# Optimization experiments

Measured on AMD Instinct MI355X. Metric: run time of the kernel, lower is better.

## Reference

```python
import jax, jax.numpy as jnp
import numpy as np

N = 100000      # nodes
E = 1600000     # edges (avg degree 16)
F_IN = 64       # input feature dim
H = 64          # hidden dim
R = 4           # relations
G = 512         # graphs in batch
C = 10          # classes
L = 3           # total conv layers (conv1 + L-1)
SCALE = 0.1


def setup_inputs() -> dict:
    key = jax.random.key(0)
    ks = jax.random.split(key, 12)
    x = jax.random.normal(ks[0], (N, F_IN), jnp.float32)
    edge_index = jax.random.randint(ks[1], (2, E), 0, N)
    edge_type = jax.random.randint(ks[2], (E,), 0, R)
    batch = jnp.sort(jax.random.randint(ks[3], (N,), 0, G))
    W1 = jax.random.normal(ks[4], (R, F_IN, H), jnp.float32) * SCALE
    root1 = jax.random.normal(ks[5], (F_IN, H), jnp.float32) * SCALE
    b1 = jnp.zeros((H,), jnp.float32)
    Wl = jax.random.normal(ks[6], (L - 1, R, H, H), jnp.float32) * SCALE
    rootl = jax.random.normal(ks[7], (L - 1, H, H), jnp.float32) * SCALE
    bl = jnp.zeros((L - 1, H), jnp.float32)
    lin1_w = jax.random.normal(ks[8], (H, H), jnp.float32) * SCALE
    lin1_b = jnp.zeros((H,), jnp.float32)
    lin2_w = jax.random.normal(ks[9], (H, C), jnp.float32) * SCALE
    lin2_b = jnp.zeros((C,), jnp.float32)
    return {"x": x, "edge_index": edge_index, "edge_type": edge_type,
            "batch": batch, "W1": W1, "root1": root1, "b1": b1,
            "Wl": Wl, "rootl": rootl, "bl": bl,
            "lin1_w": lin1_w, "lin1_b": lin1_b,
            "lin2_w": lin2_w, "lin2_b": lin2_b}


def _rgcn_conv(x, src, dst, edge_type, W, root, b):
    # Per-relation transform of all nodes (R small), then gather per edge.
    h = jnp.einsum('nd,rdf->rnf', x, W)          # [R, N, H]
    msg = h[edge_type, src]                      # [E, H] gather
    # Mean aggregation per (dst, relation): PyG RGCNConv default aggr='mean'.
    seg = dst * R + edge_type                    # combined (node, relation) id
    cnt = jax.ops.segment_sum(jnp.ones((msg.shape[0],), x.dtype), seg,
                              num_segments=x.shape[0] * R)
    norm = 1.0 / jnp.maximum(cnt[seg], 1.0)      # [E]
    agg = jax.ops.segment_sum(msg * norm[:, None], dst,
                              num_segments=x.shape[0])  # [N, H]
    return agg + x @ root + b


def _mean_pool(x, batch, num_graphs):
    s = jax.ops.segment_sum(x, batch, num_segments=num_graphs)
    cnt = jax.ops.segment_sum(jnp.ones((x.shape[0],), x.dtype), batch,
                              num_segments=num_graphs)
    return s / jnp.maximum(cnt, 1.0)[:, None]


def reference(x, edge_index, edge_type, batch, W1, root1, b1, Wl, rootl, bl,
              lin1_w, lin1_b, lin2_w, lin2_b):
    src, dst = edge_index[0], edge_index[1]
    h = jax.nn.relu(_rgcn_conv(x, src, dst, edge_type, W1, root1, b1))
    for i in range(L - 1):
        h = jax.nn.relu(_rgcn_conv(h, src, dst, edge_type, Wl[i], rootl[i], bl[i]))
    g = _mean_pool(h, batch, G)                  # [G, H]
    g = jax.nn.relu(g @ lin1_w + lin1_b)
    # dropout omitted (inference / training=False)
    return g @ lin2_w + lin2_b                   # [G, C]
```

## Files before the change

### kernel.cpp

```cpp
#include <hip/hip_runtime.h>

#define TILE 32
#define KDIM 320

typedef __attribute__((ext_vector_type(8))) short short8;
typedef __attribute__((ext_vector_type(4))) float f32x4;

__device__ inline unsigned short rne_bf16(float f) {
    union { float f; unsigned u; } x;
    x.f = f;
    unsigned r = (x.u + 0x7FFF + ((x.u >> 16) & 1)) >> 16;
    return (unsigned short)r;
}

__device__ inline float bf16_f(unsigned short v) {
    union { unsigned u; float f; } x;
    x.u = ((unsigned)v) << 16;
    return x.f;
}


__global__ void k_count(const int* __restrict__ dst, const int* __restrict__ typ,
                        int* __restrict__ cnt4, int* __restrict__ rank, int E) {
    int e = blockIdx.x * 256 + threadIdx.x;
    if (e < E) {
        int seg = dst[e] * 4 + typ[e];
        rank[e] = atomicAdd(&cnt4[seg], 1);
    }
}

__global__ void k_scan1(const int* __restrict__ in, int* __restrict__ out,
                        int* __restrict__ bsum, int M) {
    __shared__ int s[256];
    int t = threadIdx.x;
    int base = blockIdx.x * 1024 + t * 4;
    int v0 = (base + 0 < M) ? in[base + 0] : 0;
    int v1 = (base + 1 < M) ? in[base + 1] : 0;
    int v2 = (base + 2 < M) ? in[base + 2] : 0;
    int v3 = (base + 3 < M) ? in[base + 3] : 0;
    int ts = v0 + v1 + v2 + v3;
    s[t] = ts;
    __syncthreads();
    for (int off = 1; off < 256; off <<= 1) {
        int x = (t >= off) ? s[t - off] : 0;
        __syncthreads();
        s[t] += x;
        __syncthreads();
    }
    int excl = (t == 0) ? 0 : s[t - 1];
    if (t == 255) bsum[blockIdx.x] = s[255];
    if (base + 0 < M) out[base + 0] = excl;
    if (base + 1 < M) out[base + 1] = excl + v0;
    if (base + 2 < M) out[base + 2] = excl + v0 + v1;
    if (base + 3 < M) out[base + 3] = excl + v0 + v1 + v2;
}

__global__ void k_scan2(const int* __restrict__ bsum, int* __restrict__ boff, int nb) {
    __shared__ int s[512];
    int t = threadIdx.x;
    s[t] = (t < nb) ? bsum[t] : 0;
    __syncthreads();
    for (int off = 1; off < 512; off <<= 1) {
        int x = (t >= off) ? s[t - off] : 0;
        __syncthreads();
        s[t] += x;
        __syncthreads();
    }
    if (t < nb) boff[t] = (t == 0) ? 0 : s[t - 1];
}

__global__ void k_scan3(int* __restrict__ out, const int* __restrict__ boff, int M, int E) {
    int i = blockIdx.x * 256 + threadIdx.x;
    if (i < M) out[i] += boff[i >> 10];
    else if (i == M) out[M] = E;
}

__global__ void k_fill(const int* __restrict__ src, const int* __restrict__ dst,
                       const int* __restrict__ typ, const int* __restrict__ start4,
                       const int* __restrict__ rank, int* __restrict__ elist, int E) {
    int e = blockIdx.x * 256 + threadIdx.x;
    if (e < E) {
        int seg = dst[e] * 4 + typ[e];
        elist[start4[seg] + rank[e]] = src[e];
    }
}


__global__ void k_prep(const float* __restrict__ x, unsigned short* __restrict__ xb, int ncvt,
                       const float* __restrict__ W1, const float* __restrict__ root1,
                       const float* __restrict__ Wl, const float* __restrict__ rootl,
                       unsigned short* __restrict__ Wp, int nwp,
                       const int* __restrict__ batch, int* __restrict__ gstart,
                       int nN, int nG) {
    int b = blockIdx.x;
    if (b < ncvt) {
        int i = (b * 256 + threadIdx.x) * 4;
        float4 v = *reinterpret_cast<const float4*>(&x[i]);
        ushort4 o;
        o.x = rne_bf16(v.x); o.y = rne_bf16(v.y);
        o.z = rne_bf16(v.z); o.w = rne_bf16(v.w);
        *reinterpret_cast<ushort4*>(&xb[i]) = o;
        return;
    }
    b -= ncvt;
    if (b < nwp) {
        int idx = b * 256 + threadIdx.x;
        const int TOT = 3 * 320 * 64;
        if (idx >= TOT) return;
        int j = idx & 7;
        int lane = (idx >> 3) & 63;
        int t = idx >> 9;
        int ks = t % 10;
        int lnt = t / 10;
        int nt = lnt & 3;
        int layer = lnt >> 2;
        int k = ks * 32 + ((lane >> 4) << 3) + j;
        int h = nt * 16 + (lane & 15);
        float v;
        if (k < 256) {
            v = (layer == 0) ? W1[k * 64 + h] : Wl[(layer - 1) * 16384 + k * 64 + h];
        } else {
            v = (layer == 0) ? root1[(k - 256) * 64 + h]
                             : rootl[(layer - 1) * 4096 + (k - 256) * 64 + h];
        }
        Wp[idx] = rne_bf16(v);
        return;
    }
    b -= nwp;
    {
        int n = b * 256 + threadIdx.x;
        if (n >= nN) return;
        int bb = batch[n];
        if (n == 0) {
            for (int g = 0; g <= bb; ++g) gstart[g] = 0;
        } else {
            int bp = batch[n - 1];
            for (int g = bp + 1; g <= bb; ++g) gstart[g] = n;
        }
        if (n == nN - 1) {
            for (int g = bb + 1; g <= nG; ++g) gstart[g] = nN;
        }
    }
}


__global__ __launch_bounds__(256, 6) void k_conv(
        const unsigned short* __restrict__ hin, unsigned short* __restrict__ hout,
        const int* __restrict__ elist, const int* __restrict__ start4,
        const unsigned short* __restrict__ Wp, const float* __restrict__ bias, int nN) {
    __shared__ unsigned short A2[TILE * KDIM];
    const int tid = threadIdx.x;
    const int lane = tid & 63;
    const int wvs = __builtin_amdgcn_readfirstlane(tid >> 6);
    const int wv = tid >> 6;
    const int tile = blockIdx.x * TILE;

    for (int jj = 0; jj < 8; ++jj) {
        const int nl = wvs * 8 + jj;
        const int n = tile + nl;
        unsigned short* Arow = &A2[nl * KDIM];
        const int sw = (((lane >> 3) ^ (nl & 7)) << 3) + (lane & 7);
        if (n >= nN) {
#pragma unroll
            for (int seg = 0; seg < 5; ++seg) Arow[seg * 64 + sw] = 0;
            continue;
        }
        const int e0 = __builtin_amdgcn_readfirstlane(start4[n * 4 + 0]);
        const int e1 = __builtin_amdgcn_readfirstlane(start4[n * 4 + 1]);
        const int e2 = __builtin_amdgcn_readfirstlane(start4[n * 4 + 2]);
        const int e3 = __builtin_amdgcn_readfirstlane(start4[n * 4 + 3]);
        const int e4 = __builtin_amdgcn_readfirstlane(start4[n * 4 + 4]);

        unsigned short selfb = hin[((size_t)n << 6) + lane];
        float S0 = 0.f, S1 = 0.f, S2 = 0.f, S3 = 0.f;
        int p = e0;

        for (; p + 8 <= e4; p += 8) {
            int qidx[8];
#pragma unroll
            for (int u = 0; u < 8; ++u)
                qidx[u] = __builtin_amdgcn_readfirstlane(elist[p + u]);
            unsigned short vb[8];
#pragma unroll
            for (int u = 0; u < 8; ++u)
                vb[u] = hin[((size_t)qidx[u] << 6) + lane];
            __builtin_amdgcn_sched_barrier(0);
#pragma unroll
            for (int u = 0; u < 8; ++u) {
                float t = bf16_f(vb[u]);
                int q = p + u;
                S0 += t;
                S1 += (q >= e1) ? t : 0.f;
                S2 += (q >= e2) ? t : 0.f;
                S3 += (q >= e3) ? t : 0.f;
            }
        }
        if (p < e4) {
            int qidx[8];
#pragma unroll
            for (int u = 0; u < 8; ++u) {
                int q = p + u;
                int qc = (q < e4) ? q : (e4 - 1);
                qidx[u] = __builtin_amdgcn_readfirstlane(elist[qc]);
            }
            unsigned short vb[8];
#pragma unroll
            for (int u = 0; u < 8; ++u)
                vb[u] = hin[((size_t)qidx[u] << 6) + lane];
            __builtin_amdgcn_sched_barrier(0);
#pragma unroll
            for (int u = 0; u < 8; ++u) {
                int q = p + u;
                float t = (q < e4) ? bf16_f(vb[u]) : 0.f;
                S0 += t;
                S1 += (q >= e1) ? t : 0.f;
                S2 += (q >= e2) ? t : 0.f;
                S3 += (q >= e3) ? t : 0.f;
            }
        }

        int c0 = e1 - e0, c1 = e2 - e1, c2 = e3 - e2, c3 = e4 - e3;
        float a0 = (S0 - S1) * ((c0 > 0) ? 1.0f / (float)c0 : 0.f);
        float a1 = (S1 - S2) * ((c1 > 0) ? 1.0f / (float)c1 : 0.f);
        float a2 = (S2 - S3) * ((c2 > 0) ? 1.0f / (float)c2 : 0.f);
        float a3 = S3 * ((c3 > 0) ? 1.0f / (float)c3 : 0.f);
        Arow[0   + sw] = rne_bf16(a0);
        Arow[64  + sw] = rne_bf16(a1);
        Arow[128 + sw] = rne_bf16(a2);
        Arow[192 + sw] = rne_bf16(a3);
        Arow[256 + sw] = selfb;
    }
    __syncthreads();

    const int mt = wv & 1;
    const int ntb = (wv >> 1) << 1;
    const int nloc = mt * 16 + (lane & 15);
    f32x4 acc0 = {0.f, 0.f, 0.f, 0.f};
    f32x4 acc1 = {0.f, 0.f, 0.f, 0.f};
    const unsigned short* wp0 = Wp + ((size_t)(ntb * 10) * 64 + lane) * 8;
    const unsigned short* wp1 = Wp + ((size_t)((ntb + 1) * 10) * 64 + lane) * 8;
#pragma unroll 2
    for (int ks = 0; ks < 10; ++ks) {
        int kc = ks * 4 + (lane >> 4);
        int swz = (kc & ~7) | ((kc & 7) ^ (lane & 7));
        short8 a = *reinterpret_cast<const short8*>(&A2[nloc * KDIM + swz * 8]);
        short8 b0 = *reinterpret_cast<const short8*>(&wp0[ks * 512]);
        short8 b1 = *reinterpret_cast<const short8*>(&wp1[ks * 512]);
        acc0 = __builtin_amdgcn_mfma_f32_16x16x32_bf16(a, b0, acc0, 0, 0, 0);
        acc1 = __builtin_amdgcn_mfma_f32_16x16x32_bf16(a, b1, acc1, 0, 0, 0);
    }
    const int h0 = ntb * 16 + (lane & 15);
    const int nr = tile + mt * 16 + ((lane >> 4) << 2);
    const float bb0 = bias[h0];
    const float bb1 = bias[h0 + 16];
#pragma unroll
    for (int r = 0; r < 4; ++r) {
        int n = nr + r;
        if (n < nN) {
            hout[(size_t)n * 64 + h0]      = rne_bf16(fmaxf(acc0[r] + bb0, 0.f));
            hout[(size_t)n * 64 + h0 + 16] = rne_bf16(fmaxf(acc1[r] + bb1, 0.f));
        }
    }
}


__global__ void k_poolmlp(const unsigned short* __restrict__ h,
                          const int* __restrict__ gstart,
                          const float* __restrict__ w1, const float* __restrict__ b1,
                          const float* __restrict__ w2, const float* __restrict__ b2,
                          float* __restrict__ out) {
    __shared__ float red[4][64];
    __shared__ float sg[64];
    __shared__ float sh[64];
    int g = blockIdx.x;
    int t = threadIdx.x;
    int f = t & 63;
    int sl = t >> 6;
    int s = gstart[g], e = gstart[g + 1];
    float acc = 0.f;
    for (int n = s + sl; n < e; n += 4)
        acc += bf16_f(h[(size_t)n * 64 + f]);
    red[sl][f] = acc;
    __syncthreads();
    if (sl == 0) {
        int c = e - s;
        float m = (red[0][f] + red[1][f] + red[2][f] + red[3][f]) /
                  (float)((c > 0) ? c : 1);
        sg[f] = m;
    }
    __syncthreads();
    if (sl == 0) {
        float a = b1[f];
#pragma unroll 16
        for (int k = 0; k < 64; ++k) a += sg[k] * w1[k * 64 + f];
        sh[f] = fmaxf(a, 0.f);
    }
    __syncthreads();
    if (t < 10) {
        float o = b2[t];
#pragma unroll 16
        for (int k = 0; k < 64; ++k) o += sh[k] * w2[k * 10 + t];
        out[g * 10 + t] = o;
    }
}


extern "C" void kernel_launch(void* const* d_in, const int* in_sizes, int n_in,
                              void* d_out, int out_size, void* d_ws, size_t ws_size,
                              hipStream_t stream) {
    const float* x     = (const float*)d_in[0];
    const int*   ei    = (const int*)d_in[1];
    const int*   et    = (const int*)d_in[2];
    const int*   batch = (const int*)d_in[3];
    const float* W1    = (const float*)d_in[4];
    const float* root1 = (const float*)d_in[5];
    const float* b1    = (const float*)d_in[6];
    const float* Wl    = (const float*)d_in[7];
    const float* rootl = (const float*)d_in[8];
    const float* bl    = (const float*)d_in[9];
    const float* l1w   = (const float*)d_in[10];
    const float* l1b   = (const float*)d_in[11];
    const float* l2w   = (const float*)d_in[12];
    const float* l2b   = (const float*)d_in[13];
    float* out = (float*)d_out;

    const int N = in_sizes[3];
    const int E = in_sizes[2];
    const int G = out_size / 10;
    const int M = 4 * N;

    const int* src = ei;
    const int* dst = ei + E;

    char* base = (char*)d_ws;
    size_t off = 0;
    auto carve = [&](size_t bytes) {
        char* p = base + off;
        off = (off + bytes + 511) & ~(size_t)511;
        return p;
    };
    int*   cnt4    = (int*)carve((size_t)M * 4);
    int*   start4  = (int*)carve((size_t)(M + 1) * 4);
    int*   rank    = (int*)carve((size_t)E * 4);
    int*   elist   = (int*)carve((size_t)E * 4);
    int*   bsum    = (int*)carve(512 * 4);
    int*   boff    = (int*)carve(512 * 4);
    unsigned short* Wpack = (unsigned short*)carve((size_t)3 * 320 * 64 * 2);
    unsigned short* xb    = (unsigned short*)carve((size_t)N * 64 * 2);
    unsigned short* hb_a  = (unsigned short*)carve((size_t)N * 64 * 2);
    unsigned short* hb_b  = (unsigned short*)carve((size_t)N * 64 * 2);
    int*   gstart  = (int*)carve((size_t)(G + 1) * 4);
    (void)ws_size;

    hipMemsetAsync(cnt4, 0, (size_t)M * 4, stream);

    k_count<<<(E + 255) / 256, 256, 0, stream>>>(dst, et, cnt4, rank, E);

    int nb = (M + 1023) / 1024;
    k_scan1<<<nb, 256, 0, stream>>>(cnt4, start4, bsum, M);
    k_scan2<<<1, 512, 0, stream>>>(bsum, boff, nb);
    k_scan3<<<(M + 1 + 255) / 256, 256, 0, stream>>>(start4, boff, M, E);
    k_fill<<<(E + 255) / 256, 256, 0, stream>>>(src, dst, et, start4, rank, elist, E);

    const int ncvt = (N * 64 / 4 + 255) / 256;
    const int nwp  = (3 * 320 * 64 + 255) / 256;
    const int ngb  = (N + 255) / 256;
    k_prep<<<ncvt + nwp + ngb, 256, 0, stream>>>(x, xb, ncvt, W1, root1, Wl, rootl,
                                                 Wpack, nwp, batch, gstart, N, G);

    const int cb = (N + TILE - 1) / TILE;
    const int WSTRIDE = 320 * 64;
    k_conv<<<cb, 256, 0, stream>>>(xb,   hb_a, elist, start4, Wpack,               b1,      N);
    k_conv<<<cb, 256, 0, stream>>>(hb_a, hb_b, elist, start4, Wpack + WSTRIDE,     bl,      N);
    k_conv<<<cb, 256, 0, stream>>>(hb_b, hb_a, elist, start4, Wpack + 2 * WSTRIDE, bl + 64, N);

    k_poolmlp<<<G, 256, 0, stream>>>(hb_a, gstart, l1w, l1b, l2w, l2b, out);
}
```

Baseline: 344.5 us.

## Double-buffer edge gathers in conv, merge count into prep kernel

The neighbor gather loop in k_conv becomes software-pipelined. It issues 16 loads per batch into two alternating register buffers, so the next batch's loads are in flight while the current batch is accumulated. Relation masks now use scalar readfirstlane-derived multipliers with fma instead of selects. The edge-count atomic kernel is folded into k_prep to save a launch, and k_conv launch bounds are raised to 8 waves per SIMD. The larger register buffers could conflict with the tighter occupancy bound and cause spills.

```diff
diff --git a/kernel.cpp b/kernel.cpp
--- a/kernel.cpp
+++ b/kernel.cpp
@@ -19,15 +19,63 @@
     return x.f;
 }
 
-
-__global__ void k_count(const int* __restrict__ dst, const int* __restrict__ typ,
-                        int* __restrict__ cnt4, int* __restrict__ rank, int E) {
-    int e = blockIdx.x * 256 + threadIdx.x;
-    if (e < E) {
-        int seg = dst[e] * 4 + typ[e];
-        rank[e] = atomicAdd(&cnt4[seg], 1);
-    }
-}
+#define SMASK(cond) __int_as_float(__builtin_amdgcn_readfirstlane((cond) ? 0x3f800000 : 0))
+
+#define ISSUE_FULL(P, Q, V)                                                    \
+    do {                                                                       \
+        _Pragma("unroll") for (int u = 0; u < 16; ++u)                         \
+            Q[u] = __builtin_amdgcn_readfirstlane(elist[(P) + u]);             \
+        _Pragma("unroll") for (int u = 0; u < 16; ++u)                         \
+            V[u] = hin[((size_t)Q[u] << 6) + lane];                            \
+    } while (0)
+
+#define ISSUE_PRED(P, Q, V)                                                    \
+    do {                                                                       \
+        _Pragma("unroll") for (int u = 0; u < 16; ++u) {                       \
+            int q_ = (P) + u;                                                  \
+            int qc_ = (q_ < e4) ? q_ : (e4 - 1);                               \
+            Q[u] = __builtin_amdgcn_readfirstlane(elist[qc_]);                 \
+        }                                                                      \
+        _Pragma("unroll") for (int u = 0; u < 16; ++u)                         \
+            V[u] = hin[((size_t)Q[u] << 6) + lane];                            \
+    } while (0)
+
+#define ISSUE_ANY(P, Q, V)                                                     \
+    do {                                                                       \
+        if ((P) + 16 <= e4) ISSUE_FULL(P, Q, V);                               \
+        else ISSUE_PRED(P, Q, V);                                              \
+    } while (0)
+
+#define CONSUME_FULL(P, V)                                                     \
+    do {                                                                       \
+        _Pragma("unroll") for (int u = 0; u < 16; ++u) {                       \
+            float t_ = bf16_f(V[u]);                                           \
+            int q_ = (P) + u;                                                  \
+            S0 += t_;                                                          \
+            S1 = fmaf(t_, SMASK(q_ >= e1), S1);                                \
+            S2 = fmaf(t_, SMASK(q_ >= e2), S2);                                \
+            S3 = fmaf(t_, SMASK(q_ >= e3), S3);                                \
+        }                                                                      \
+    } while (0)
+
+#define CONSUME_PRED(P, V)                                                     \
+    do {                                                                       \
+        _Pragma("unroll") for (int u = 0; u < 16; ++u) {                       \
+            int q_ = (P) + u;                                                  \
+            float t_ = bf16_f(V[u]) * SMASK(q_ < e4);                          \
+            S0 += t_;                                                          \
+            S1 = fmaf(t_, SMASK(q_ >= e1), S1);                                \
+            S2 = fmaf(t_, SMASK(q_ >= e2), S2);                                \
+            S3 = fmaf(t_, SMASK(q_ >= e3), S3);                                \
+        }                                                                      \
+    } while (0)
+
+#define CONSUME_ANY(P, V)                                                      \
+    do {                                                                       \
+        if ((P) + 16 <= e4) CONSUME_FULL(P, V);                                \
+        else CONSUME_PRED(P, V);                                               \
+    } while (0)
+
 
 __global__ void k_scan1(const int* __restrict__ in, int* __restrict__ out,
                         int* __restrict__ bsum, int M) {
@@ -86,13 +134,24 @@
 }
 
 
-__global__ void k_prep(const float* __restrict__ x, unsigned short* __restrict__ xb, int ncvt,
+__global__ void k_prep(const int* __restrict__ dst, const int* __restrict__ typ,
+                       int* __restrict__ cnt4, int* __restrict__ rank, int E, int necnt,
+                       const float* __restrict__ x, unsigned short* __restrict__ xb, int ncvt,
                        const float* __restrict__ W1, const float* __restrict__ root1,
                        const float* __restrict__ Wl, const float* __restrict__ rootl,
                        unsigned short* __restrict__ Wp, int nwp,
                        const int* __restrict__ batch, int* __restrict__ gstart,
                        int nN, int nG) {
     int b = blockIdx.x;
+    if (b < necnt) {
+        int e = b * 256 + threadIdx.x;
+        if (e < E) {
+            int seg = dst[e] * 4 + typ[e];
+            rank[e] = atomicAdd(&cnt4[seg], 1);
+        }
+        return;
+    }
+    b -= necnt;
     if (b < ncvt) {
         int i = (b * 256 + threadIdx.x) * 4;
         float4 v = *reinterpret_cast<const float4*>(&x[i]);
@@ -144,7 +203,7 @@
 }
 
 
-__global__ __launch_bounds__(256, 6) void k_conv(
+__global__ __launch_bounds__(256, 8) void k_conv(
         const unsigned short* __restrict__ hin, unsigned short* __restrict__ hout,
         const int* __restrict__ elist, const int* __restrict__ start4,
         const unsigned short* __restrict__ Wp, const float* __restrict__ bias, int nN) {
@@ -173,49 +232,26 @@
 
         unsigned short selfb = hin[((size_t)n << 6) + lane];
         float S0 = 0.f, S1 = 0.f, S2 = 0.f, S3 = 0.f;
-        int p = e0;
-
-        for (; p + 8 <= e4; p += 8) {
-            int qidx[8];
-#pragma unroll
-            for (int u = 0; u < 8; ++u)
-                qidx[u] = __builtin_amdgcn_readfirstlane(elist[p + u]);
-            unsigned short vb[8];
-#pragma unroll
-            for (int u = 0; u < 8; ++u)
-                vb[u] = hin[((size_t)qidx[u] << 6) + lane];
-            __builtin_amdgcn_sched_barrier(0);
-#pragma unroll
-            for (int u = 0; u < 8; ++u) {
-                float t = bf16_f(vb[u]);
-                int q = p + u;
-                S0 += t;
-                S1 += (q >= e1) ? t : 0.f;
-                S2 += (q >= e2) ? t : 0.f;
-                S3 += (q >= e3) ? t : 0.f;
-            }
-        }
-        if (p < e4) {
-            int qidx[8];
-#pragma unroll
-            for (int u = 0; u < 8; ++u) {
-                int q = p + u;
-                int qc = (q < e4) ? q : (e4 - 1);
-                qidx[u] = __builtin_amdgcn_readfirstlane(elist[qc]);
-            }
-            unsigned short vb[8];
-#pragma unroll
-            for (int u = 0; u < 8; ++u)
-                vb[u] = hin[((size_t)qidx[u] << 6) + lane];
-            __builtin_amdgcn_sched_barrier(0);
-#pragma unroll
-            for (int u = 0; u < 8; ++u) {
-                int q = p + u;
-                float t = (q < e4) ? bf16_f(vb[u]) : 0.f;
-                S0 += t;
-                S1 += (q >= e1) ? t : 0.f;
-                S2 += (q >= e2) ? t : 0.f;
-                S3 += (q >= e3) ? t : 0.f;
+
+        if (e0 < e4) {
+            int qA[16], qB[16];
+            unsigned short vA[16], vB[16];
+            int p = e0;
+            ISSUE_ANY(p, qA, vA);
+            bool useA = true;
+            while (p < e4) {
+                int pn = p + 16;
+                if (useA) {
+                    if (pn < e4) ISSUE_ANY(pn, qB, vB);
+                    __builtin_amdgcn_sched_barrier(0);
+                    CONSUME_ANY(p, vA);
+                } else {
+                    if (pn < e4) ISSUE_ANY(pn, qA, vA);
+                    __builtin_amdgcn_sched_barrier(0);
+                    CONSUME_ANY(p, vB);
+                }
+                p = pn;
+                useA = !useA;
             }
         }
 
@@ -354,7 +390,14 @@
 
     hipMemsetAsync(cnt4, 0, (size_t)M * 4, stream);
 
-    k_count<<<(E + 255) / 256, 256, 0, stream>>>(dst, et, cnt4, rank, E);
+    const int necnt = (E + 255) / 256;
+    const int ncvt = (N * 64 / 4 + 255) / 256;
+    const int nwp  = (3 * 320 * 64 + 255) / 256;
+    const int ngb  = (N + 255) / 256;
+    k_prep<<<necnt + ncvt + nwp + ngb, 256, 0, stream>>>(
+        dst, et, cnt4, rank, E, necnt,
+        x, xb, ncvt, W1, root1, Wl, rootl, Wpack, nwp,
+        batch, gstart, N, G);
 
     int nb = (M + 1023) / 1024;
     k_scan1<<<nb, 256, 0, stream>>>(cnt4, start4, bsum, M);
@@ -362,12 +405,6 @@
     k_scan3<<<(M + 1 + 255) / 256, 256, 0, stream>>>(start4, boff, M, E);
     k_fill<<<(E + 255) / 256, 256, 0, stream>>>(src, dst, et, start4, rank, elist, E);
 
-    const int ncvt = (N * 64 / 4 + 255) / 256;
-    const int nwp  = (3 * 320 * 64 + 255) / 256;
-    const int ngb  = (N + 255) / 256;
-    k_prep<<<ncvt + nwp + ngb, 256, 0, stream>>>(x, xb, ncvt, W1, root1, Wl, rootl,
-                                                 Wpack, nwp, batch, gstart, N, G);
-
     const int cb = (N + TILE - 1) / TILE;
     const int WSTRIDE = 320 * 64;
     k_conv<<<cb, 256, 0, stream>>>(xb,   hb_a, elist, start4, Wpack,               b1,      N);
```

Result: slower. 403.9 us (+17.2%).

## Gather neighbor rows as 4-lane vectors across 4 edge groups, fuse count into prep

Applied to the files above, without the earlier changes.

The edge-gather loop in the conv kernel now spreads four edges at a time across lane groups. Each lane loads a 4-element bf16 vector (8 bytes) of a neighbor row instead of one element per lane per edge, and the per-relation sums are combined with cross-lane shuffle reductions before the LDS write. This aims to cut the number of memory instructions per gathered row and keep more loads in flight per edge. In exchange it adds 16 accumulators, shuffle reductions and masked work on tail edges. Separately, the atomic edge-count kernel is merged into the prep kernel launch to save one kernel launch.

```diff
diff --git a/kernel.cpp b/kernel.cpp
--- a/kernel.cpp
+++ b/kernel.cpp
@@ -19,15 +19,6 @@
     return x.f;
 }
 
-
-__global__ void k_count(const int* __restrict__ dst, const int* __restrict__ typ,
-                        int* __restrict__ cnt4, int* __restrict__ rank, int E) {
-    int e = blockIdx.x * 256 + threadIdx.x;
-    if (e < E) {
-        int seg = dst[e] * 4 + typ[e];
-        rank[e] = atomicAdd(&cnt4[seg], 1);
-    }
-}
 
 __global__ void k_scan1(const int* __restrict__ in, int* __restrict__ out,
                         int* __restrict__ bsum, int M) {
@@ -86,13 +77,24 @@
 }
 
 
-__global__ void k_prep(const float* __restrict__ x, unsigned short* __restrict__ xb, int ncvt,
+__global__ void k_prep(const int* __restrict__ dst, const int* __restrict__ typ,
+                       int* __restrict__ cnt4, int* __restrict__ rank, int E, int necnt,
+                       const float* __restrict__ x, unsigned short* __restrict__ xb, int ncvt,
                        const float* __restrict__ W1, const float* __restrict__ root1,
                        const float* __restrict__ Wl, const float* __restrict__ rootl,
                        unsigned short* __restrict__ Wp, int nwp,
                        const int* __restrict__ batch, int* __restrict__ gstart,
                        int nN, int nG) {
     int b = blockIdx.x;
+    if (b < necnt) {
+        int e = b * 256 + threadIdx.x;
+        if (e < E) {
+            int seg = dst[e] * 4 + typ[e];
+            rank[e] = atomicAdd(&cnt4[seg], 1);
+        }
+        return;
+    }
+    b -= necnt;
     if (b < ncvt) {
         int i = (b * 256 + threadIdx.x) * 4;
         float4 v = *reinterpret_cast<const float4*>(&x[i]);
@@ -144,6 +146,31 @@
 }
 
 
+#define CONSUME4(I, D)                                                         \
+    do {                                                                       \
+        float m0 = ((I) < e4) ? 1.f : 0.f;                                     \
+        float m1 = ((I) >= e1) ? 1.f : 0.f;                                    \
+        float m2 = ((I) >= e2) ? 1.f : 0.f;                                    \
+        float m3 = ((I) >= e3) ? 1.f : 0.f;                                    \
+        float t0 = bf16_f((D).x) * m0;                                         \
+        float t1 = bf16_f((D).y) * m0;                                         \
+        float t2 = bf16_f((D).z) * m0;                                         \
+        float t3 = bf16_f((D).w) * m0;                                         \
+        s00 += t0; s01 += t1; s02 += t2; s03 += t3;                            \
+        s10 = fmaf(t0, m1, s10); s11 = fmaf(t1, m1, s11);                      \
+        s12 = fmaf(t2, m1, s12); s13 = fmaf(t3, m1, s13);                      \
+        s20 = fmaf(t0, m2, s20); s21 = fmaf(t1, m2, s21);                      \
+        s22 = fmaf(t2, m2, s22); s23 = fmaf(t3, m2, s23);                      \
+        s30 = fmaf(t0, m3, s30); s31 = fmaf(t1, m3, s31);                      \
+        s32 = fmaf(t2, m3, s32); s33 = fmaf(t3, m3, s33);                      \
+    } while (0)
+
+#define RED2(v)                                                                \
+    do {                                                                       \
+        v += __shfl_xor(v, 16, 64);                                            \
+        v += __shfl_xor(v, 32, 64);                                            \
+    } while (0)
+
 __global__ __launch_bounds__(256, 6) void k_conv(
         const unsigned short* __restrict__ hin, unsigned short* __restrict__ hout,
         const int* __restrict__ elist, const int* __restrict__ start4,
@@ -155,6 +182,9 @@
     const int wv = tid >> 6;
     const int tile = blockIdx.x * TILE;
 
+    const int eg = lane >> 4;
+    const int fo = (lane & 15) * 4;
+
     for (int jj = 0; jj < 8; ++jj) {
         const int nl = wvs * 8 + jj;
         const int n = tile + nl;
@@ -172,62 +202,79 @@
         const int e4 = __builtin_amdgcn_readfirstlane(start4[n * 4 + 4]);
 
         unsigned short selfb = hin[((size_t)n << 6) + lane];
-        float S0 = 0.f, S1 = 0.f, S2 = 0.f, S3 = 0.f;
-        int p = e0;
-
-        for (; p + 8 <= e4; p += 8) {
-            int qidx[8];
-#pragma unroll
-            for (int u = 0; u < 8; ++u)
-                qidx[u] = __builtin_amdgcn_readfirstlane(elist[p + u]);
-            unsigned short vb[8];
-#pragma unroll
-            for (int u = 0; u < 8; ++u)
-                vb[u] = hin[((size_t)qidx[u] << 6) + lane];
+        float s00 = 0.f, s01 = 0.f, s02 = 0.f, s03 = 0.f;
+        float s10 = 0.f, s11 = 0.f, s12 = 0.f, s13 = 0.f;
+        float s20 = 0.f, s21 = 0.f, s22 = 0.f, s23 = 0.f;
+        float s30 = 0.f, s31 = 0.f, s32 = 0.f, s33 = 0.f;
+
+        for (int p = e0; p < e4; p += 16) {
+            int i0 = p + 0 + eg;
+            int i1 = p + 4 + eg;
+            int i2 = p + 8 + eg;
+            int i3 = p + 12 + eg;
+            int c0 = (i0 < e4) ? i0 : (e4 - 1);
+            int c1 = (i1 < e4) ? i1 : (e4 - 1);
+            int c2 = (i2 < e4) ? i2 : (e4 - 1);
+            int c3 = (i3 < e4) ? i3 : (e4 - 1);
+            int x0 = elist[c0];
+            int x1 = elist[c1];
+            int x2 = elist[c2];
+            int x3 = elist[c3];
+            ushort4 d0 = *reinterpret_cast<const ushort4*>(&hin[((size_t)x0 << 6) + fo]);
+            ushort4 d1 = *reinterpret_cast<const ushort4*>(&hin[((size_t)x1 << 6) + fo]);
+            ushort4 d2 = *reinterpret_cast<const ushort4*>(&hin[((size_t)x2 << 6) + fo]);
+            ushort4 d3 = *reinterpret_cast<const ushort4*>(&hin[((size_t)x3 << 6) + fo]);
             __builtin_amdgcn_sched_barrier(0);
-#pragma unroll
-            for (int u = 0; u < 8; ++u) {
-                float t = bf16_f(vb[u]);
-                int q = p + u;
-                S0 += t;
-                S1 += (q >= e1) ? t : 0.f;
-                S2 += (q >= e2) ? t : 0.f;
-                S3 += (q >= e3) ? t : 0.f;
+            CONSUME4(i0, d0);
+            CONSUME4(i1, d1);
+            CONSUME4(i2, d2);
+            CONSUME4(i3, d3);
+        }
+
+        RED2(s00); RED2(s01); RED2(s02); RED2(s03);
+        RED2(s10); RED2(s11); RED2(s12); RED2(s13);
+        RED2(s20); RED2(s21); RED2(s22); RED2(s23);
+        RED2(s30); RED2(s31); RED2(s32); RED2(s33);
+
+        int cA = e1 - e0, cB = e2 - e1, cC = e3 - e2, cD = e4 - e3;
+        float iA = (cA > 0) ? 1.0f / (float)cA : 0.f;
+        float iB = (cB > 0) ? 1.0f / (float)cB : 0.f;
+        float iC = (cC > 0) ? 1.0f / (float)cC : 0.f;
+        float iD = (cD > 0) ? 1.0f / (float)cD : 0.f;
+
+        if (lane < 16) {
+            const int half = lane & 1;
+            const int kcs = lane >> 1;
+            ushort4 w;
+            w.x = rne_bf16((s00 - s10) * iA); w.y = rne_bf16((s01 - s11) * iA);
+            w.z = rne_bf16((s02 - s12) * iA); w.w = rne_bf16((s03 - s13) * iA);
+            {
+                int kc = 0 * 8 + kcs;
+                int off = ((kc & ~7) + ((kc & 7) ^ (nl & 7))) * 8 + half * 4;
+                *reinterpret_cast<ushort4*>(&Arow[off]) = w;
             }
-        }
-        if (p < e4) {
-            int qidx[8];
-#pragma unroll
-            for (int u = 0; u < 8; ++u) {
-                int q = p + u;
-                int qc = (q < e4) ? q : (e4 - 1);
-                qidx[u] = __builtin_amdgcn_readfirstlane(elist[qc]);
+            w.x = rne_bf16((s10 - s20) * iB); w.y = rne_bf16((s11 - s21) * iB);
+            w.z = rne_bf16((s12 - s22) * iB); w.w = rne_bf16((s13 - s23) * iB);
+            {
+                int kc = 1 * 8 + kcs;
+                int off = ((kc & ~7) + ((kc & 7) ^ (nl & 7))) * 8 + half * 4;
+                *reinterpret_cast<ushort4*>(&Arow[off]) = w;
             }
-            unsigned short vb[8];
-#pragma unroll
-            for (int u = 0; u < 8; ++u)
-                vb[u] = hin[((size_t)qidx[u] << 6) + lane];
-            __builtin_amdgcn_sched_barrier(0);
-#pragma unroll
-            for (int u = 0; u < 8; ++u) {
-                int q = p + u;
-                float t = (q < e4) ? bf16_f(vb[u]) : 0.f;
-                S0 += t;
-                S1 += (q >= e1) ? t : 0.f;
-                S2 += (q >= e2) ? t : 0.f;
-                S3 += (q >= e3) ? t : 0.f;
+            w.x = rne_bf16((s20 - s30) * iC); w.y = rne_bf16((s21 - s31) * iC);
+            w.z = rne_bf16((s22 - s32) * iC); w.w = rne_bf16((s23 - s33) * iC);
+            {
+                int kc = 2 * 8 + kcs;
+                int off = ((kc & ~7) + ((kc & 7) ^ (nl & 7))) * 8 + half * 4;
+                *reinterpret_cast<ushort4*>(&Arow[off]) = w;
             }
-        }
-
-        int c0 = e1 - e0, c1 = e2 - e1, c2 = e3 - e2, c3 = e4 - e3;
-        float a0 = (S0 - S1) * ((c0 > 0) ? 1.0f / (float)c0 : 0.f);
-        float a1 = (S1 - S2) * ((c1 > 0) ? 1.0f / (float)c1 : 0.f);
-        float a2 = (S2 - S3) * ((c2 > 0) ? 1.0f / (float)c2 : 0.f);
-        float a3 = S3 * ((c3 > 0) ? 1.0f / (float)c3 : 0.f);
-        Arow[0   + sw] = rne_bf16(a0);
-        Arow[64  + sw] = rne_bf16(a1);
-        Arow[128 + sw] = rne_bf16(a2);
-        Arow[192 + sw] = rne_bf16(a3);
+            w.x = rne_bf16(s30 * iD); w.y = rne_bf16(s31 * iD);
+            w.z = rne_bf16(s32 * iD); w.w = rne_bf16(s33 * iD);
+            {
+                int kc = 3 * 8 + kcs;
+                int off = ((kc & ~7) + ((kc & 7) ^ (nl & 7))) * 8 + half * 4;
+                *reinterpret_cast<ushort4*>(&Arow[off]) = w;
+            }
+        }
         Arow[256 + sw] = selfb;
     }
     __syncthreads();
@@ -354,7 +401,14 @@
 
     hipMemsetAsync(cnt4, 0, (size_t)M * 4, stream);
 
-    k_count<<<(E + 255) / 256, 256, 0, stream>>>(dst, et, cnt4, rank, E);
+    const int necnt = (E + 255) / 256;
+    const int ncvt = (N * 64 / 4 + 255) / 256;
+    const int nwp  = (3 * 320 * 64 + 255) / 256;
+    const int ngb  = (N + 255) / 256;
+    k_prep<<<necnt + ncvt + nwp + ngb, 256, 0, stream>>>(
+        dst, et, cnt4, rank, E, necnt,
+        x, xb, ncvt, W1, root1, Wl, rootl, Wpack, nwp,
+        batch, gstart, N, G);
 
     int nb = (M + 1023) / 1024;
     k_scan1<<<nb, 256, 0, stream>>>(cnt4, start4, bsum, M);
@@ -362,12 +416,6 @@
     k_scan3<<<(M + 1 + 255) / 256, 256, 0, stream>>>(start4, boff, M, E);
     k_fill<<<(E + 255) / 256, 256, 0, stream>>>(src, dst, et, start4, rank, elist, E);
 
-    const int ncvt = (N * 64 / 4 + 255) / 256;
-    const int nwp  = (3 * 320 * 64 + 255) / 256;
-    const int ngb  = (N + 255) / 256;
-    k_prep<<<ncvt + nwp + ngb, 256, 0, stream>>>(x, xb, ncvt, W1, root1, Wl, rootl,
-                                                 Wpack, nwp, batch, gstart, N, G);
-
     const int cb = (N + TILE - 1) / TILE;
     const int WSTRIDE = 320 * 64;
     k_conv<<<cb, 256, 0, stream>>>(xb,   hb_a, elist, start4, Wpack,               b1,      N);
```

New measurement: 339.4 us. About the same (-1.5%).
